# Kernel tuning notes

Measured on AMD Instinct MI355X. Metric: run time of the kernel, lower is better.

## Reference

```python
import jax, jax.numpy as jnp
import numpy as np
from jax import lax

NFFT = 1747        # round(fs/resolution) = round(512/0.293)
FFT_START = 24     # round(7/0.293)
FFT_END = 240      # round(70/0.293)+1
TEMP = 30.0        # softmax temperature of DynamicConv attention
EPS = 1e-5         # BatchNorm eps


def transform(x):
    # x: (B,1,Chans,T) -> FFT features (B,1,Chans,432), no grad in original
    samples = x.shape[-1]
    X = jnp.fft.rfft(x, n=NFFT, axis=-1) / samples
    real = X.real[..., FFT_START:FFT_END]
    imag = X.imag[..., FFT_START:FFT_END]
    return jnp.concatenate([real, imag], axis=-1).astype(jnp.float32)


def dyn_conv(x, wk, a1w, a1b, a2w, a2b, dilation):
    # x: (B,Cin,H,W); wk: (K,Cout,Cin,kh,kw)
    p = x.mean(axis=(2, 3))                              # global avg pool (B,Cin)
    h = jax.nn.relu(p @ a1w.T + a1b)                     # (B,hidden)
    att = jax.nn.softmax((h @ a2w.T + a2b) / TEMP, -1)   # (B,K)
    w = jnp.einsum('bk,koihw->boihw', att, wk)           # per-sample kernels

    def per_sample(xi, wi):
        return lax.conv_general_dilated(
            xi[None], wi, (1, 1), 'VALID', rhs_dilation=dilation,
            dimension_numbers=('NCHW', 'OIHW', 'NCHW'))[0]

    return jax.vmap(per_sample)(x, w)                    # grouped conv, groups=B


def batchnorm(x, g, b):
    m = x.mean(axis=(0, 2, 3), keepdims=True)
    v = x.var(axis=(0, 2, 3), keepdims=True)
    return g[None, :, None, None] * (x - m) * jax.lax.rsqrt(v + EPS) + b[None, :, None, None]


def setup_inputs() -> dict:
    key = jax.random.key(0)
    ks = jax.random.split(key, 8)
    B, Chans, T = 4096, 8, 512
    K, F, OUTW, NCLS = 4, 16, 405, 4
    s = 0.01  # init std in init_weights
    x = jax.random.normal(ks[0], (B, Chans, T), jnp.float32)
    w1k = s * jax.random.normal(ks[1], (K, F, 1, Chans, 1), jnp.float32)
    a1w1 = s * jax.random.normal(ks[2], (1, 1), jnp.float32)
    a1b1 = jnp.zeros((1,), jnp.float32)
    a1w2 = s * jax.random.normal(ks[3], (K, 1), jnp.float32)
    a1b2 = jnp.zeros((K,), jnp.float32)
    g1 = jnp.ones((F,), jnp.float32); b1 = jnp.zeros((F,), jnp.float32)
    w2k = s * jax.random.normal(ks[4], (K, F, F, 1, 10), jnp.float32)
    a2w1 = s * jax.random.normal(ks[5], (F // 4, F), jnp.float32)
    a2b1 = jnp.zeros((F // 4,), jnp.float32)
    a2w2 = s * jax.random.normal(ks[6], (K, F // 4), jnp.float32)
    a2b2 = jnp.zeros((K,), jnp.float32)
    g2 = jnp.ones((F,), jnp.float32); b2 = jnp.zeros((F,), jnp.float32)
    fcw = s * jax.random.normal(ks[7], (NCLS, F * OUTW), jnp.float32)
    fcb = jnp.zeros((NCLS,), jnp.float32)
    return dict(x=x, w1k=w1k, a1w1=a1w1, a1b1=a1b1, a1w2=a1w2, a1b2=a1b2,
                g1=g1, b1=b1, w2k=w2k, a2w1=a2w1, a2b1=a2b1, a2w2=a2w2,
                a2b2=a2b2, g2=g2, b2=b2, fcw=fcw, fcb=fcb)


def reference(x, w1k, a1w1, a1b1, a1w2, a1b2, g1, b1,
              w2k, a2w1, a2b1, a2w2, a2b2, g2, b2, fcw, fcb):
    h = x[:, None]                                   # (B,1,Chans,T)
    h = lax.stop_gradient(transform(h))              # (B,1,8,432)
    h = jax.nn.relu(batchnorm(dyn_conv(h, w1k, a1w1, a1b1, a1w2, a1b2, (1, 1)), g1, b1))  # (B,16,1,432)
    h = jax.nn.relu(batchnorm(dyn_conv(h, w2k, a2w1, a2b1, a2w2, a2b2, (1, 3)), g2, b2))  # (B,16,1,405)
    h = h.reshape(h.shape[0], -1)                    # (B,6480)
    return h @ fcw.T + fcb                           # (B,4)
```

## Files before the change

kernel.cpp:

```cpp
#include <hip/hip_runtime.h>
#include <math.h>

#define NB   216
#define W1   432
#define W2   405
#define NSAMP 4096
#define NFFTC 1747

typedef __bf16 bf16x8 __attribute__((ext_vector_type(8)));
typedef float  f32x4  __attribute__((ext_vector_type(4)));
typedef unsigned int u32x4 __attribute__((ext_vector_type(4)));
typedef unsigned int u32x2 __attribute__((ext_vector_type(2)));

__device__ __forceinline__ unsigned int bfbits(float f) {
    return (unsigned int)__builtin_bit_cast(unsigned short, (__bf16)f);
}
__device__ __forceinline__ float bf2f(unsigned int u) {
    return (float)__builtin_bit_cast(__bf16, (unsigned short)(u & 0xffff));
}

__global__ __launch_bounds__(256) void k_prep(unsigned short* __restrict__ basf,
        const float* __restrict__ fcw, unsigned int* __restrict__ fcwp,
        const float* __restrict__ w2k, float* __restrict__ w2kT) {
    int blk = blockIdx.x, tid = threadIdx.x;
    if (blk < 112) {
        int g = blk * 256 + tid;
        int lane = g & 63;
        int kq = (g >> 6) & 15;
        int nt = g >> 10;
        int w  = nt * 16 + (lane & 15);
        int t0 = kq * 32 + (lane >> 4) * 8;
        unsigned int p[4] = {0u, 0u, 0u, 0u};
        if (w < W1) {
            int k = (w < NB) ? (24 + w) : (w - 192);
            #pragma unroll
            for (int e = 0; e < 8; ++e) {
                int m = (k * (t0 + e)) % NFFTC;
                float ang = (float)m * (float)(6.283185307179586 / 1747.0);
                float c = (w < NB) ? cosf(ang) : -sinf(ang);
                unsigned int bits = bfbits(c * (1.f / 512.f));
                p[e >> 1] |= bits << ((e & 1) * 16);
            }
        }
        u32x4 v = {p[0], p[1], p[2], p[3]};
        *(u32x4*)(basf + (size_t)g * 8) = v;
    } else if (blk < 125) {
        int p = (blk - 112) * 256 + tid;
        if (p < 3240) {
            int idx0 = 2 * p;
            int w = idx0 >> 4, oc = idx0 & 15;
            unsigned int r[4];
            #pragma unroll
            for (int h = 0; h < 2; ++h) {
                int c = oc + h;
                float n0 = fcw[0 * 6480 + c * W2 + w];
                float n1 = fcw[1 * 6480 + c * W2 + w];
                float n2 = fcw[2 * 6480 + c * W2 + w];
                float n3 = fcw[3 * 6480 + c * W2 + w];
                r[2 * h]     = bfbits(n0) | (bfbits(n1) << 16);
                r[2 * h + 1] = bfbits(n2) | (bfbits(n3) << 16);
            }
            ((u32x4*)fcwp)[p] = (u32x4){r[0], r[1], r[2], r[3]};
        }
    } else {
        int idx = (blk - 125) * 256 + tid;
        if (idx < 10240) {
            int k = idx / 2560, rem = idx - k * 2560;
            int oc = rem / 160, r2 = rem - oc * 160;
            int tp = r2 >> 4, ic = r2 & 15;
            w2kT[idx] = w2k[((k * 16 + oc) * 16 + ic) * 10 + tp];
        }
    }
}

__global__ __launch_bounds__(256, 4) void k_fused(const float* __restrict__ x,
        const unsigned short* __restrict__ basf,
        const float* __restrict__ w1k, const float* __restrict__ a1w1,
        const float* __restrict__ a1b1, const float* __restrict__ a1w2,
        const float* __restrict__ a1b2,
        unsigned short* __restrict__ C1, float* __restrict__ part1) {
    __shared__ __attribute__((aligned(16))) unsigned short Al[17920];
    __shared__ float ps[4][4];
    int tid = threadIdx.x, blk = blockIdx.x;
    int wv = tid >> 6, lane = tid & 63;
    int cq = wv;
    int kg = lane >> 4, col16 = lane & 15;

    {
        const float* xrow = x + (size_t)(blk * 32 + (tid >> 7) * 16 + (lane & 15)) * 512
                              + ((tid >> 6) & 1) * 32 + (lane >> 4) * 8;
        #pragma unroll
        for (int i = 0; i < 8; ++i) {
            f32x4 a = *(const f32x4*)(xrow + i * 64);
            f32x4 b = *(const f32x4*)(xrow + i * 64 + 4);
            u32x4 v;
            v[0] = bfbits(a[0]) | (bfbits(a[1]) << 16);
            v[1] = bfbits(a[2]) | (bfbits(a[3]) << 16);
            v[2] = bfbits(b[0]) | (bfbits(b[1]) << 16);
            v[3] = bfbits(b[2]) | (bfbits(b[3]) << 16);
            *(u32x4*)&Al[(size_t)(tid + 256 * i) * 8] = v;
        }
    }
    __syncthreads();

    f32x4 acc[2][7];
    #pragma unroll
    for (int rh = 0; rh < 2; ++rh)
        #pragma unroll
        for (int j = 0; j < 7; ++j) acc[rh][j] = (f32x4){0.f, 0.f, 0.f, 0.f};
    #pragma unroll
    for (int kq = 0; kq < 16; ++kq) {
        bf16x8 fa0 = *(const bf16x8*)&Al[(((kq >> 1) * 4 + 0 + (kq & 1)) * 64 + lane) * 8];
        bf16x8 fa1 = *(const bf16x8*)&Al[(((kq >> 1) * 4 + 2 + (kq & 1)) * 64 + lane) * 8];
        #pragma unroll
        for (int j = 0; j < 7; ++j) {
            bf16x8 fb = *(const bf16x8*)(basf + (size_t)(((cq * 7 + j) * 16 + kq) * 64 + lane) * 8);
            acc[0][j] = __builtin_amdgcn_mfma_f32_16x16x32_bf16(fa0, fb, acc[0][j], 0, 0, 0);
            acc[1][j] = __builtin_amdgcn_mfma_f32_16x16x32_bf16(fa1, fb, acc[1][j], 0, 0, 0);
        }
    }

    {
        float s0 = 0.f, s1 = 0.f;
        #pragma unroll
        for (int j = 0; j < 7; ++j)
            #pragma unroll
            for (int e = 0; e < 4; ++e) { s0 += acc[0][j][e]; s1 += acc[1][j][e]; }
        #pragma unroll
        for (int m = 1; m < 32; m <<= 1) { s0 += __shfl_xor(s0, m); s1 += __shfl_xor(s1, m); }
        if ((lane & 31) == 0) {
            int hi = lane >> 5;
            ps[wv][hi] = s0;
            ps[wv][2 + hi] = s1;
        }
    }
    __syncthreads();

    #pragma unroll
    for (int rh = 0; rh < 2; ++rh)
        #pragma unroll
        for (int j = 0; j < 7; ++j) {
            int col = cq * 112 + j * 16 + col16;
            u32x2 pk;
            pk[0] = bfbits(acc[rh][j][0]) | (bfbits(acc[rh][j][1]) << 16);
            pk[1] = bfbits(acc[rh][j][2]) | (bfbits(acc[rh][j][3]) << 16);
            *(u32x2*)&Al[col * 40 + rh * 16 + kg * 4] = pk;
        }
    __syncthreads();

    int s = wv;
    float p1 = (ps[0][s] + ps[1][s] + ps[2][s] + ps[3][s]) * (1.f / (8.f * W1));
    float h = fmaxf(p1 * a1w1[0] + a1b1[0], 0.f);
    float l[4], mx = -1e30f;
    #pragma unroll
    for (int k = 0; k < 4; ++k) { l[k] = (h * a1w2[k] + a1b2[k]) * (1.f / 30.f); mx = fmaxf(mx, l[k]); }
    float es = 0.f;
    #pragma unroll
    for (int k = 0; k < 4; ++k) { l[k] = expf(l[k] - mx); es += l[k]; }
    float inv = 1.f / es;
    float at[4] = {l[0] * inv, l[1] * inv, l[2] * inv, l[3] * inv};

    int q = lane >> 4, i = lane & 15;
    float kr[4][8];
    #pragma unroll
    for (int c = 0; c < 4; ++c)
        #pragma unroll
        for (int ch = 0; ch < 8; ++ch) {
            float kv = 0.f;
            #pragma unroll
            for (int k = 0; k < 4; ++k)
                kv = fmaf(at[k], w1k[k * 128 + (q * 4 + c) * 8 + ch], kv);
            kr[c][ch] = kv;
        }
    int b = blk * 4 + s;
    unsigned short* c1o = C1 + (size_t)b * (432 * 16);
    float ssum[4] = {}, ssq[4] = {};
    for (int pass = 0; pass < 27; ++pass) {
        int w = i + 16 * pass;
        bf16x8 y8 = *(const bf16x8*)&Al[w * 40 + s * 8];
        float yf[8];
        #pragma unroll
        for (int ch = 0; ch < 8; ++ch) yf[ch] = (float)y8[ch];
        u32x2 pk = {0u, 0u};
        #pragma unroll
        for (int c = 0; c < 4; ++c) {
            float a = 0.f;
            #pragma unroll
            for (int ch = 0; ch < 8; ++ch) a = fmaf(kr[c][ch], yf[ch], a);
            ssum[c] += a; ssq[c] = fmaf(a, a, ssq[c]);
            pk[c >> 1] |= bfbits(a) << ((c & 1) * 16);
        }
        *(u32x2*)&c1o[w * 16 + q * 4] = pk;
    }
    #pragma unroll
    for (int m = 1; m < 16; m <<= 1)
        #pragma unroll
        for (int c = 0; c < 4; ++c) { ssum[c] += __shfl_xor(ssum[c], m); ssq[c] += __shfl_xor(ssq[c], m); }
    if (i == 0) {
        #pragma unroll
        for (int c = 0; c < 4; ++c) {
            part1[(q * 4 + c) * NSAMP + b] = ssum[c];
            part1[(16 + q * 4 + c) * NSAMP + b] = ssq[c];
        }
    }
}

__global__ __launch_bounds__(256) void k_statfin2(const float* __restrict__ part,
        const float* __restrict__ g, const float* __restrict__ bb,
        float* __restrict__ ss, float cnt) {
    __shared__ float red[2][4];
    int i = blockIdx.x, tid = threadIdx.x;
    const f32x4* psr = (const f32x4*)(part + (size_t)i * NSAMP);
    const f32x4* qs = (const f32x4*)(part + (size_t)(16 + i) * NSAMP);
    float s = 0.f, q = 0.f;
    #pragma unroll
    for (int jj = 0; jj < 4; ++jj) {
        int j = tid + jj * 256;
        f32x4 a = psr[j], c = qs[j];
        s += a[0] + a[1] + a[2] + a[3];
        q += c[0] + c[1] + c[2] + c[3];
    }
    #pragma unroll
    for (int m = 32; m; m >>= 1) { s += __shfl_xor(s, m); q += __shfl_xor(q, m); }
    if ((tid & 63) == 0) { red[0][tid >> 6] = s; red[1][tid >> 6] = q; }
    __syncthreads();
    if (tid == 0) {
        float sum = red[0][0] + red[0][1] + red[0][2] + red[0][3];
        float sq  = red[1][0] + red[1][1] + red[1][2] + red[1][3];
        float mean = sum / cnt;
        float var  = sq / cnt - mean * mean;
        float sc = g[i] * rsqrtf(var + 1e-5f);
        ss[i] = sc;
        ss[16 + i] = bb[i] - mean * sc;
    }
}

#define H1T_STR 24
#define H1T_ROWS 448
__global__ __launch_bounds__(256) void k_conv2(const unsigned short* __restrict__ C1b,
        const float* __restrict__ w2kT, const float* __restrict__ a2w1,
        const float* __restrict__ a2b1, const float* __restrict__ a2w2,
        const float* __restrict__ a2b2, const float* __restrict__ ss,
        unsigned short* __restrict__ H2Tb, float* __restrict__ part2) {
    __shared__ __attribute__((aligned(16))) unsigned short H1T[H1T_ROWS * H1T_STR];
    __shared__ __attribute__((aligned(16))) unsigned short Bl[16 * 160];
    __shared__ float p2p[4][16];
    __shared__ float sred[4][2][16];
    int b = blockIdx.x, tid = threadIdx.x;
    int wv = tid >> 6, lane = tid & 63;

    for (int w = tid; w < W1; w += 256) {
        const u32x4* src = (const u32x4*)(C1b + ((size_t)b * W1 + w) * 16);
        u32x4 v0 = src[0], v1 = src[1];
        unsigned int op[8];
        #pragma unroll
        for (int i = 0; i < 8; ++i) {
            unsigned int u = (i < 4) ? v0[i] : v1[i - 4];
            float a = fmaxf(fmaf(bf2f(u),       ss[2*i],     ss[16 + 2*i]),     0.f);
            float c = fmaxf(fmaf(bf2f(u >> 16), ss[2*i + 1], ss[16 + 2*i + 1]), 0.f);
            op[i] = bfbits(a) | (bfbits(c) << 16);
        }
        *(u32x4*)&H1T[w * H1T_STR]     = (u32x4){op[0], op[1], op[2], op[3]};
        *(u32x4*)&H1T[w * H1T_STR + 8] = (u32x4){op[4], op[5], op[6], op[7]};
    }
    if (tid < 128) {
        int r = 432 + (tid >> 3), c = (tid & 7) * 2;
        *(unsigned int*)&H1T[r * H1T_STR + c] = 0u;
    }
    __syncthreads();

    {
        int chn = tid & 15, seg = tid >> 4;
        float s = 0.f;
        for (int j = 0; j < 27; ++j)
            s += bf2f((unsigned int)H1T[(seg * 27 + j) * H1T_STR + chn]);
        s += __shfl_xor(s, 16);
        s += __shfl_xor(s, 32);
        if ((lane & 48) == 0) p2p[wv][chn] = s;
    }
    __syncthreads();

    float hv[4];
    #pragma unroll
    for (int j = 0; j < 4; ++j) {
        float a = a2b1[j];
        #pragma unroll
        for (int i = 0; i < 16; ++i) {
            float p2 = (p2p[0][i] + p2p[1][i] + p2p[2][i] + p2p[3][i]) * (1.f / (float)W1);
            a = fmaf(a2w1[j * 16 + i], p2, a);
        }
        hv[j] = fmaxf(a, 0.f);
    }
    float l[4], mx = -1e30f;
    #pragma unroll
    for (int k = 0; k < 4; ++k) {
        float a = a2b2[k];
        #pragma unroll
        for (int j = 0; j < 4; ++j) a = fmaf(a2w2[k * 4 + j], hv[j], a);
        l[k] = a * (1.f / 30.f); mx = fmaxf(mx, l[k]);
    }
    float es = 0.f;
    #pragma unroll
    for (int k = 0; k < 4; ++k) { l[k] = expf(l[k] - mx); es += l[k]; }
    float inv = 1.f / es;
    float at0 = l[0] * inv, at1 = l[1] * inv, at2 = l[2] * inv, at3 = l[3] * inv;
    #pragma unroll
    for (int i = 0; i < 10; ++i) {
        int idx = tid + i * 256;
        float v = at0 * w2kT[idx] + at1 * w2kT[2560 + idx]
                + at2 * w2kT[5120 + idx] + at3 * w2kT[7680 + idx];
        Bl[idx] = (unsigned short)bfbits(v);
    }
    __syncthreads();

    int col = lane & 15, kg = lane >> 4;
    bf16x8 bfrag[5];
    #pragma unroll
    for (int s = 0; s < 5; ++s)
        bfrag[s] = *(const bf16x8*)&Bl[col * 160 + s * 32 + kg * 8];
    float s2 = 0.f, q2 = 0.f;
    for (int mt = wv; mt < 26; mt += 4) {
        int wbase = mt * 16;
        f32x4 acc = {0.f, 0.f, 0.f, 0.f};
        #pragma unroll
        for (int s = 0; s < 5; ++s) {
            int tp = 2 * s + (kg >> 1);
            int row = wbase + col + 3 * tp;
            bf16x8 a = *(const bf16x8*)&H1T[row * H1T_STR + (kg & 1) * 8];
            acc = __builtin_amdgcn_mfma_f32_16x16x32_bf16(a, bfrag[s], acc, 0, 0, 0);
        }
        unsigned short* hb = H2Tb + (size_t)b * (16 * W2) + (wbase + kg * 4) * 16 + col;
        #pragma unroll
        for (int r = 0; r < 4; ++r) {
            int w = wbase + kg * 4 + r;
            if (w < W2) {
                float v = acc[r];
                hb[r * 16] = (unsigned short)bfbits(v);
                s2 += v; q2 = fmaf(v, v, q2);
            }
        }
    }
    s2 += __shfl_xor(s2, 16); q2 += __shfl_xor(q2, 16);
    s2 += __shfl_xor(s2, 32); q2 += __shfl_xor(q2, 32);
    if (lane < 16) { sred[wv][0][lane] = s2; sred[wv][1][lane] = q2; }
    __syncthreads();
    if (tid < 16) {
        part2[tid * NSAMP + b] = sred[0][0][tid] + sred[1][0][tid] + sred[2][0][tid] + sred[3][0][tid];
    } else if (tid < 32) {
        int i = tid - 16;
        part2[(16 + i) * NSAMP + b] = sred[0][1][i] + sred[1][1][i] + sred[2][1][i] + sred[3][1][i];
    }
}

__global__ __launch_bounds__(256) void k_fc(const unsigned short* __restrict__ H2Tb,
        const float* __restrict__ ss2, const unsigned int* __restrict__ fcwp,
        const float* __restrict__ fcb, float* __restrict__ out) {
    __shared__ float red[4][4];
    int b = blockIdx.x, tid = threadIdx.x;
    const unsigned int* hb = (const unsigned int*)(H2Tb + (size_t)b * (16 * W2));
    const u32x4* fw = (const u32x4*)fcwp;
    float acc[4] = {};
    for (int p = tid; p < 3240; p += 256) {
        unsigned int u = hb[p];
        int oc = (2 * p) & 15;
        float v0 = fmaxf(fmaf(bf2f(u),       ss2[oc],     ss2[16 + oc]),     0.f);
        float v1 = fmaxf(fmaf(bf2f(u >> 16), ss2[oc + 1], ss2[16 + oc + 1]), 0.f);
        u32x4 wv4 = fw[p];
        acc[0] = fmaf(v0, bf2f(wv4[0]),       fmaf(v1, bf2f(wv4[2]),       acc[0]));
        acc[1] = fmaf(v0, bf2f(wv4[0] >> 16), fmaf(v1, bf2f(wv4[2] >> 16), acc[1]));
        acc[2] = fmaf(v0, bf2f(wv4[1]),       fmaf(v1, bf2f(wv4[3]),       acc[2]));
        acc[3] = fmaf(v0, bf2f(wv4[1] >> 16), fmaf(v1, bf2f(wv4[3] >> 16), acc[3]));
    }
    #pragma unroll
    for (int m = 1; m < 64; m <<= 1)
        #pragma unroll
        for (int n = 0; n < 4; ++n) acc[n] += __shfl_xor(acc[n], m);
    int wid = tid >> 6, lane = tid & 63;
    if (lane == 0) {
        #pragma unroll
        for (int n = 0; n < 4; ++n) red[wid][n] = acc[n];
    }
    __syncthreads();
    if (tid < 4)
        out[b * 4 + tid] = red[0][tid] + red[1][tid] + red[2][tid] + red[3][tid] + fcb[tid];
}

extern "C" void kernel_launch(void* const* d_in, const int* in_sizes, int n_in,
                              void* d_out, int out_size, void* d_ws, size_t ws_size,
                              hipStream_t stream) {
    const float* x    = (const float*)d_in[0];
    const float* w1k  = (const float*)d_in[1];
    const float* a1w1 = (const float*)d_in[2];
    const float* a1b1 = (const float*)d_in[3];
    const float* a1w2 = (const float*)d_in[4];
    const float* a1b2 = (const float*)d_in[5];
    const float* g1   = (const float*)d_in[6];
    const float* b1   = (const float*)d_in[7];
    const float* w2k  = (const float*)d_in[8];
    const float* a2w1 = (const float*)d_in[9];
    const float* a2b1 = (const float*)d_in[10];
    const float* a2w2 = (const float*)d_in[11];
    const float* a2b2 = (const float*)d_in[12];
    const float* g2   = (const float*)d_in[13];
    const float* b2   = (const float*)d_in[14];
    const float* fcw  = (const float*)d_in[15];
    const float* fcb  = (const float*)d_in[16];

    float* ws = (float*)d_ws;
    unsigned short* H2Tb = (unsigned short*)ws;
    float*          part1 = ws + 14155776;
    float*          part2 = part1 + 32 * NSAMP;
    float*          w2kT  = part2 + 32 * NSAMP;
    unsigned int*   fcwp  = (unsigned int*)(w2kT + 10240);
    unsigned short* C1b  = (unsigned short*)(ws + 26542080);
    unsigned short* basf = (unsigned short*)(ws + 26542080 + 14155776);
    float* ssf   = ws + 26542080 + 14155776 + 114688;

    k_prep<<<165, 256, 0, stream>>>(basf, fcw, fcwp, w2k, w2kT);
    k_fused<<<1024, 256, 0, stream>>>(x, basf, w1k, a1w1, a1b1, a1w2, a1b2, C1b, part1);
    k_statfin2<<<16, 256, 0, stream>>>(part1, g1, b1, ssf, 4096.f * 432.f);
    k_conv2<<<NSAMP, 256, 0, stream>>>(C1b, w2kT, a2w1, a2b1, a2w2, a2b2, ssf, H2Tb, part2);
    k_statfin2<<<16, 256, 0, stream>>>(part2, g2, b2, ssf + 32, 4096.f * 405.f);
    k_fc<<<NSAMP, 256, 0, stream>>>(H2Tb, ssf + 32, fcwp, fcb, (float*)d_out);
}
```

Baseline: 112.9 us.

## Use MFMA for conv1 channel mix and restructure FC with LDS-cached weights

The first conv's 8→16 channel mixing per sample moves from scalar FMAs to a 16x16x32 bf16 MFMA. The A fragment holds the attention-combined kernel and is zero-padded outside the valid k group. Separately, the FC kernel now processes 8 samples per 512-thread block, one wave per sample. The packed FC weights are staged once per block into padded LDS arrays, which removes the cross-wave reduction. Risks are the correctness of the fragment lane mapping, and the large LDS footprint lowering FC occupancy.

```diff
diff --git a/kernel.cpp b/kernel.cpp
--- a/kernel.cpp
+++ b/kernel.cpp
@@ -160,47 +160,38 @@
     float inv = 1.f / es;
     float at[4] = {l[0] * inv, l[1] * inv, l[2] * inv, l[3] * inv};
 
-    int q = lane >> 4, i = lane & 15;
-    float kr[4][8];
-    #pragma unroll
-    for (int c = 0; c < 4; ++c)
-        #pragma unroll
-        for (int ch = 0; ch < 8; ++ch) {
-            float kv = 0.f;
-            #pragma unroll
-            for (int k = 0; k < 4; ++k)
-                kv = fmaf(at[k], w1k[k * 128 + (q * 4 + c) * 8 + ch], kv);
-            kr[c][ch] = kv;
-        }
+    bf16x8 afrag;
+    #pragma unroll
+    for (int ch = 0; ch < 8; ++ch) {
+        float kv = 0.f;
+        #pragma unroll
+        for (int k = 0; k < 4; ++k) kv = fmaf(at[k], w1k[k * 128 + col16 * 8 + ch], kv);
+        afrag[ch] = (kg == 0) ? (__bf16)kv : (__bf16)0.f;
+    }
     int b = blk * 4 + s;
     unsigned short* c1o = C1 + (size_t)b * (432 * 16);
     float ssum[4] = {}, ssq[4] = {};
-    for (int pass = 0; pass < 27; ++pass) {
-        int w = i + 16 * pass;
-        bf16x8 y8 = *(const bf16x8*)&Al[w * 40 + s * 8];
-        float yf[8];
-        #pragma unroll
-        for (int ch = 0; ch < 8; ++ch) yf[ch] = (float)y8[ch];
-        u32x2 pk = {0u, 0u};
+    #pragma unroll 3
+    for (int wt = 0; wt < 27; ++wt) {
+        bf16x8 bfrag = *(const bf16x8*)&Al[(wt * 16 + col16) * 40 + s * 8];
+        f32x4 d = {0.f, 0.f, 0.f, 0.f};
+        d = __builtin_amdgcn_mfma_f32_16x16x32_bf16(afrag, bfrag, d, 0, 0, 0);
+        u32x2 pk;
+        pk[0] = bfbits(d[0]) | (bfbits(d[1]) << 16);
+        pk[1] = bfbits(d[2]) | (bfbits(d[3]) << 16);
+        *(u32x2*)&c1o[(wt * 16 + col16) * 16 + kg * 4] = pk;
+        #pragma unroll
+        for (int i = 0; i < 4; ++i) { ssum[i] += d[i]; ssq[i] = fmaf(d[i], d[i], ssq[i]); }
+    }
+    #pragma unroll
+    for (int m = 1; m < 16; m <<= 1)
+        #pragma unroll
+        for (int c = 0; c < 4; ++c) { ssum[c] += __shfl_xor(ssum[c], m); ssq[c] += __shfl_xor(ssq[c], m); }
+    if (col16 == 0) {
         #pragma unroll
         for (int c = 0; c < 4; ++c) {
-            float a = 0.f;
-            #pragma unroll
-            for (int ch = 0; ch < 8; ++ch) a = fmaf(kr[c][ch], yf[ch], a);
-            ssum[c] += a; ssq[c] = fmaf(a, a, ssq[c]);
-            pk[c >> 1] |= bfbits(a) << ((c & 1) * 16);
-        }
-        *(u32x2*)&c1o[w * 16 + q * 4] = pk;
-    }
-    #pragma unroll
-    for (int m = 1; m < 16; m <<= 1)
-        #pragma unroll
-        for (int c = 0; c < 4; ++c) { ssum[c] += __shfl_xor(ssum[c], m); ssq[c] += __shfl_xor(ssq[c], m); }
-    if (i == 0) {
-        #pragma unroll
-        for (int c = 0; c < 4; ++c) {
-            part1[(q * 4 + c) * NSAMP + b] = ssum[c];
-            part1[(16 + q * 4 + c) * NSAMP + b] = ssq[c];
+            part1[(kg * 4 + c) * NSAMP + b] = ssum[c];
+            part1[(16 + kg * 4 + c) * NSAMP + b] = ssq[c];
         }
     }
 }
@@ -352,37 +343,38 @@
     }
 }
 
-__global__ __launch_bounds__(256) void k_fc(const unsigned short* __restrict__ H2Tb,
+__global__ __launch_bounds__(512) void k_fc(const unsigned short* __restrict__ H2Tb,
         const float* __restrict__ ss2, const unsigned int* __restrict__ fcwp,
         const float* __restrict__ fcb, float* __restrict__ out) {
-    __shared__ float red[4][4];
-    int b = blockIdx.x, tid = threadIdx.x;
+    __shared__ u32x2 flo[3443], fhi[3443];
+    int tid = threadIdx.x, wv = tid >> 6, lane = tid & 63;
+    for (int p = tid; p < 3240; p += 512) {
+        u32x4 v = ((const u32x4*)fcwp)[p];
+        int pi = p + (p >> 4);
+        flo[pi] = (u32x2){v[0], v[1]};
+        fhi[pi] = (u32x2){v[2], v[3]};
+    }
+    __syncthreads();
+    int b = blockIdx.x * 8 + wv;
     const unsigned int* hb = (const unsigned int*)(H2Tb + (size_t)b * (16 * W2));
-    const u32x4* fw = (const u32x4*)fcwp;
     float acc[4] = {};
-    for (int p = tid; p < 3240; p += 256) {
+    for (int p = lane; p < 3240; p += 64) {
         unsigned int u = hb[p];
         int oc = (2 * p) & 15;
         float v0 = fmaxf(fmaf(bf2f(u),       ss2[oc],     ss2[16 + oc]),     0.f);
         float v1 = fmaxf(fmaf(bf2f(u >> 16), ss2[oc + 1], ss2[16 + oc + 1]), 0.f);
-        u32x4 wv4 = fw[p];
-        acc[0] = fmaf(v0, bf2f(wv4[0]),       fmaf(v1, bf2f(wv4[2]),       acc[0]));
-        acc[1] = fmaf(v0, bf2f(wv4[0] >> 16), fmaf(v1, bf2f(wv4[2] >> 16), acc[1]));
-        acc[2] = fmaf(v0, bf2f(wv4[1]),       fmaf(v1, bf2f(wv4[3]),       acc[2]));
-        acc[3] = fmaf(v0, bf2f(wv4[1] >> 16), fmaf(v1, bf2f(wv4[3] >> 16), acc[3]));
+        int pi = p + (p >> 4);
+        u32x2 lo = flo[pi], hi = fhi[pi];
+        acc[0] = fmaf(v0, bf2f(lo[0]),       fmaf(v1, bf2f(hi[0]),       acc[0]));
+        acc[1] = fmaf(v0, bf2f(lo[0] >> 16), fmaf(v1, bf2f(hi[0] >> 16), acc[1]));
+        acc[2] = fmaf(v0, bf2f(lo[1]),       fmaf(v1, bf2f(hi[1]),       acc[2]));
+        acc[3] = fmaf(v0, bf2f(lo[1] >> 16), fmaf(v1, bf2f(hi[1] >> 16), acc[3]));
     }
     #pragma unroll
     for (int m = 1; m < 64; m <<= 1)
         #pragma unroll
         for (int n = 0; n < 4; ++n) acc[n] += __shfl_xor(acc[n], m);
-    int wid = tid >> 6, lane = tid & 63;
-    if (lane == 0) {
-        #pragma unroll
-        for (int n = 0; n < 4; ++n) red[wid][n] = acc[n];
-    }
-    __syncthreads();
-    if (tid < 4)
-        out[b * 4 + tid] = red[0][tid] + red[1][tid] + red[2][tid] + red[3][tid] + fcb[tid];
+    if (lane < 4) out[b * 4 + lane] = acc[lane] + fcb[lane];
 }
 
 extern "C" void kernel_launch(void* const* d_in, const int* in_sizes, int n_in,
@@ -421,5 +413,5 @@
     k_statfin2<<<16, 256, 0, stream>>>(part1, g1, b1, ssf, 4096.f * 432.f);
     k_conv2<<<NSAMP, 256, 0, stream>>>(C1b, w2kT, a2w1, a2b1, a2w2, a2b2, ssf, H2Tb, part2);
     k_statfin2<<<16, 256, 0, stream>>>(part2, g2, b2, ssf + 32, 4096.f * 405.f);
-    k_fc<<<NSAMP, 256, 0, stream>>>(H2Tb, ssf + 32, fcwp, fcb, (float*)d_out);
-}
+    k_fc<<<NSAMP / 8, 512, 0, stream>>>(H2Tb, ssf + 32, fcwp, fcb, (float*)d_out);
+}
```

New measurement: 106.0 us. 1.07x faster.
